# Kernel tuning notes

Hardware: AMD Instinct MI355X
Metric: run time of the kernel (lower is better)

## Reference

```python
import jax, jax.numpy as jnp
import numpy as np

N_NODES = 100000
N_EDGES = 1000000
N_GRAPHS = 512
HID = 64
EDIM = 32
LAYERS = 4
BN_EPS = 1e-5


def _batchnorm(x, g, b):
    # training-mode BatchNorm1d: biased batch statistics over the node axis
    m = x.mean(axis=0)
    v = jnp.var(x, axis=0)
    return (x - m) * jax.lax.rsqrt(v + BN_EPS) * g + b


def setup_inputs() -> dict:
    key = jax.random.key(0)
    ks = jax.random.split(key, 16)
    zw = 2 * HID + EDIM  # 160: cat([x_i, x_j, e_ij])
    inp = {
        "z": jax.random.randint(ks[0], (N_NODES,), 0, 100),
        "edge_index": jax.random.randint(ks[1], (2, N_EDGES), 0, N_NODES),
        "edge_attr": jax.random.normal(ks[2], (N_EDGES, EDIM), dtype=jnp.float32),
        "batch_ids": jnp.sort(jax.random.randint(ks[3], (N_NODES,), 0, N_GRAPHS)),
        "emb": jax.random.normal(ks[4], (100, HID), dtype=jnp.float32),
        "Wf": jax.random.normal(ks[5], (LAYERS, zw, HID), dtype=jnp.float32) / np.sqrt(zw),
        "bf": jnp.zeros((LAYERS, HID), jnp.float32),
        "Ws": jax.random.normal(ks[6], (LAYERS, zw, HID), dtype=jnp.float32) / np.sqrt(zw),
        "bs": jnp.zeros((LAYERS, HID), jnp.float32),
        "g_cbn": jnp.ones((LAYERS, HID), jnp.float32),
        "b_cbn": jnp.zeros((LAYERS, HID), jnp.float32),
        "g_obn": jnp.ones((LAYERS, HID), jnp.float32),
        "b_obn": jnp.zeros((LAYERS, HID), jnp.float32),
        "W1": jax.random.normal(ks[7], (HID, HID), dtype=jnp.float32) / np.sqrt(HID),
        "b1": jnp.zeros((HID,), jnp.float32),
        "W2": jax.random.normal(ks[8], (HID, 1), dtype=jnp.float32) / np.sqrt(HID),
        "b2": jnp.zeros((1,), jnp.float32),
    }
    return inp


def reference(z, edge_index, edge_attr, batch_ids, emb, Wf, bf, Ws, bs,
              g_cbn, b_cbn, g_obn, b_obn, W1, b1, W2, b2):
    src = edge_index[0]  # x_j (source)
    dst = edge_index[1]  # x_i (target / aggregation index)
    x = emb[z]  # [N, HID]
    for l in range(LAYERS):
        # CGConv message: z_e = cat([x_i, x_j, e_ij]); m = sigmoid(f(z_e)) * softplus(s(z_e))
        z_e = jnp.concatenate([x[dst], x[src], edge_attr], axis=-1)  # [E, 160]
        msg = jax.nn.sigmoid(z_e @ Wf[l] + bf[l]) * jax.nn.softplus(z_e @ Ws[l] + bs[l])
        agg = jax.ops.segment_sum(msg, dst, num_segments=N_NODES)  # [N, HID]
        agg = _batchnorm(agg, g_cbn[l], b_cbn[l])  # CGConv's internal BN
        x = agg + x  # residual
        x = _batchnorm(x, g_obn[l], b_obn[l])  # outer BatchNorm1d
        x = jax.nn.softplus(x)
    # global mean pool over graphs
    sums = jax.ops.segment_sum(x, batch_ids, num_segments=N_GRAPHS)
    cnts = jax.ops.segment_sum(jnp.ones((N_NODES,), x.dtype), batch_ids, num_segments=N_GRAPHS)
    pooled = sums / jnp.maximum(cnts, 1.0)[:, None]
    h = jax.nn.silu(pooled @ W1 + b1)  # dropout is identity in eval mode
    out = (h @ W2 + b2)[:, 0]
    return out
```

## Files before the change

### kernel.cpp

```cpp
#include <hip/hip_runtime.h>
#include <cstdint>
#include <cstddef>

#define N_NODES 100000
#define N_EDGES 1000000
#define N_GRAPHS 512
#define HID 64
#define EDIM 32
#define LAYERS 4
#define BN_EPS 1e-5

static const size_t X_OFF    = 0;
static const size_t AGG_OFF  = X_OFF + 25600000;
static const size_t STA_OFF  = AGG_OFF + 25600000;
static const size_t STB_OFF  = STA_OFF + 1024;
static const size_t POOL_OFF = STB_OFF + 1024;
static const size_t CNT_OFF  = POOL_OFF + 131072;
static const size_t DEG_OFF  = CNT_OFF + 2048;
static const size_t ECUR_OFF = DEG_OFF + 400128;
static const size_t PERM_OFF = ECUR_OFF + 400128;
static const size_t DSTS_OFF = PERM_OFF + 4000000;
static const size_t BSUM_OFF = DSTS_OFF + 4000000;
static const size_t BOFF_OFF = BSUM_OFF + 2048;
static const size_t P_OFF    = BOFF_OFF + 2048;

#define SCAN_BLOCKS 391

__device__ __forceinline__ float rl_f(float v, int k) {
    return __uint_as_float(__builtin_amdgcn_readlane(__float_as_uint(v), k));
}
__device__ __forceinline__ float sigmoidf_(float x) {
    return 1.f / (1.f + __expf(-x));
}
__device__ __forceinline__ float softplusf_(float x) {
    return fmaxf(x, 0.f) + __logf(1.f + __expf(-fabsf(x)));
}
__device__ __forceinline__ void fma4(float4& a, const float4& wv, float xv) {
    a.x = fmaf(xv, wv.x, a.x);
    a.y = fmaf(xv, wv.y, a.y);
    a.z = fmaf(xv, wv.z, a.z);
    a.w = fmaf(xv, wv.w, a.w);
}

__global__ __launch_bounds__(256) void cg_embed(const int* __restrict__ z,
                                                const float* __restrict__ emb,
                                                float* __restrict__ x) {
    int i = blockIdx.x * 256 + threadIdx.x;
    if (i < N_NODES * HID) {
        x[i] = emb[z[i >> 6] * HID + (i & 63)];
    }
}

__global__ __launch_bounds__(256) void cg_hist(const int* __restrict__ ei,
                                               int* __restrict__ deg) {
    int e = blockIdx.x * 256 + threadIdx.x;
    if (e < N_EDGES) atomicAdd(&deg[ei[N_EDGES + e]], 1);
}

__global__ __launch_bounds__(256) void cg_bsum(const int* __restrict__ deg,
                                               int* __restrict__ bsum) {
    const int i = blockIdx.x * 256 + threadIdx.x;
    int v = (i < N_NODES) ? deg[i] : 0;
#pragma unroll
    for (int off = 32; off > 0; off >>= 1) v += __shfl_down(v, off);
    __shared__ int wsum[4];
    if ((threadIdx.x & 63) == 0) wsum[threadIdx.x >> 6] = v;
    __syncthreads();
    if (threadIdx.x == 0) bsum[blockIdx.x] = wsum[0] + wsum[1] + wsum[2] + wsum[3];
}

__global__ __launch_bounds__(512) void cg_bscan(const int* __restrict__ bsum,
                                                int* __restrict__ boff) {
    __shared__ int ps[512];
    const int t = threadIdx.x;
    int v = (t < SCAN_BLOCKS) ? bsum[t] : 0;
    ps[t] = v;
    __syncthreads();
    for (int off = 1; off < 512; off <<= 1) {
        int u = (t >= off) ? ps[t - off] : 0;
        __syncthreads();
        ps[t] += u;
        __syncthreads();
    }
    if (t < SCAN_BLOCKS) boff[t] = ps[t] - v;
}

__global__ __launch_bounds__(256) void cg_escan(const int* __restrict__ deg,
                                                const int* __restrict__ boff,
                                                int* __restrict__ ecur) {
    __shared__ int ps[256];
    const int t = threadIdx.x;
    const int i = blockIdx.x * 256 + t;
    int v = (i < N_NODES) ? deg[i] : 0;
    ps[t] = v;
    __syncthreads();
    for (int off = 1; off < 256; off <<= 1) {
        int u = (t >= off) ? ps[t - off] : 0;
        __syncthreads();
        ps[t] += u;
        __syncthreads();
    }
    if (i < N_NODES) ecur[i] = ps[t] - v + boff[blockIdx.x];
}

__global__ __launch_bounds__(256) void cg_scatter(const int* __restrict__ ei,
                                                  int* __restrict__ ecur,
                                                  int* __restrict__ perm,
                                                  int* __restrict__ dst_s) {
    int e = blockIdx.x * 256 + threadIdx.x;
    if (e < N_EDGES) {
        int d = ei[N_EDGES + e];
        int pos = atomicAdd(&ecur[d], 1);
        perm[pos] = e;
        dst_s[pos] = d;
    }
}

__global__ __launch_bounds__(256, 4) void cg_nodeP4(const float* __restrict__ x,
                                                    const float* __restrict__ Wf,
                                                    const float* __restrict__ Ws,
                                                    float* __restrict__ P) {
    __shared__ __align__(16) float xs[64][68];
    const int tid = threadIdx.x;
    const int base = blockIdx.x * 64;
#pragma unroll
    for (int i = 0; i < 4; i++) {
        int f4 = tid * 4 + i;
        int r = f4 >> 4, c4 = (f4 & 15) * 4;
        float4 v = {0, 0, 0, 0};
        if (base + r < N_NODES) v = *(const float4*)(x + (size_t)(base + r) * HID + c4);
        *(float4*)(&xs[r][c4]) = v;
    }
    __syncthreads();

    const int g = tid >> 4;
    const int j4 = (tid & 15) * 4;
    float4 acc[4][4];
#pragma unroll
    for (int m = 0; m < 4; m++)
#pragma unroll
        for (int q = 0; q < 4; q++) acc[m][q] = {0, 0, 0, 0};

    for (int k = 0; k < 64; k++) {
        float4 w0 = *(const float4*)(Wf + (size_t)k * HID + j4);
        float4 w1 = *(const float4*)(Ws + (size_t)k * HID + j4);
        float4 w2 = *(const float4*)(Wf + (size_t)(64 + k) * HID + j4);
        float4 w3 = *(const float4*)(Ws + (size_t)(64 + k) * HID + j4);
#pragma unroll
        for (int m = 0; m < 4; m++) {
            float xv = xs[g + m * 16][k];
            fma4(acc[m][0], w0, xv);
            fma4(acc[m][1], w1, xv);
            fma4(acc[m][2], w2, xv);
            fma4(acc[m][3], w3, xv);
        }
    }
#pragma unroll
    for (int m = 0; m < 4; m++) {
        int r = base + g + m * 16;
        if (r < N_NODES) {
            float* o = P + (size_t)r * 256;
            *(float4*)(o + j4)       = acc[m][0];
            *(float4*)(o + 64 + j4)  = acc[m][1];
            *(float4*)(o + 128 + j4) = acc[m][2];
            *(float4*)(o + 192 + j4) = acc[m][3];
        }
    }
}

__global__ __launch_bounds__(256, 4) void cg_edge3(const float* __restrict__ P,
                                                   const int* __restrict__ ei,
                                                   const float* __restrict__ ea,
                                                   const int* __restrict__ perm,
                                                   const int* __restrict__ dst_s,
                                                   const float* __restrict__ WfE,
                                                   const float* __restrict__ WsE,
                                                   const float* __restrict__ bf,
                                                   const float* __restrict__ bs,
                                                   float* __restrict__ agg) {
    const int j = threadIdx.x & 63;
    float wfe[EDIM], wse[EDIM];
#pragma unroll
    for (int k = 0; k < EDIM; k++) {
        wfe[k] = WfE[k * HID + j];
        wse[k] = WsE[k * HID + j];
    }
    const float bfv = bf[j], bsv = bs[j];
    const int wave = blockIdx.x * 4 + (threadIdx.x >> 6);
    const int nw = gridDim.x * 4;
    const int chunk = (N_EDGES + nw - 1) / nw;
    const int e0 = wave * chunk;
    const int e1 = min(e0 + chunk, N_EDGES);
    if (e0 >= e1) return;

    int cur = __builtin_amdgcn_readfirstlane(dst_s[e0]);
    float pf0 = P[(size_t)cur * 256 + j];
    float ps0 = P[(size_t)cur * 256 + 64 + j];
    float acc = 0.f;

    for (int e = e0; e < e1; ++e) {
        const int d  = __builtin_amdgcn_readfirstlane(dst_s[e]);
        const int pe = __builtin_amdgcn_readfirstlane(perm[e]);
        if (d != cur) {
            unsafeAtomicAdd(&agg[(size_t)cur * HID + j], acc);
            acc = 0.f;
            cur = d;
            pf0 = P[(size_t)cur * 256 + j];
            ps0 = P[(size_t)cur * 256 + 64 + j];
        }
        const int s = __builtin_amdgcn_readfirstlane(ei[pe]);
        const float sf = P[(size_t)s * 256 + 128 + j];
        const float ss = P[(size_t)s * 256 + 192 + j];
        const float* __restrict__ earow = ea + (size_t)pe * EDIM;
        float uf = bfv + pf0 + sf;
        float us = bsv + ps0 + ss;
#pragma unroll
        for (int k = 0; k < EDIM; k++) {
            const float ek = earow[k];
            uf = fmaf(ek, wfe[k], uf);
            us = fmaf(ek, wse[k], us);
        }
        acc += sigmoidf_(uf) * softplusf_(us);
    }
    unsafeAtomicAdd(&agg[(size_t)cur * HID + j], acc);
}

__global__ __launch_bounds__(256) void cg_stats(const float* __restrict__ a,
                                                double* __restrict__ stA,
                                                double* __restrict__ stB) {
    if (blockIdx.x == 0 && threadIdx.x < 128) stB[threadIdx.x] = 0.0;
    const int j = threadIdx.x & 63, rl = threadIdx.x >> 6;
    float s = 0.f, q = 0.f;
    for (int n = blockIdx.x * 4 + rl; n < N_NODES; n += gridDim.x * 4) {
        float v = a[(size_t)n * HID + j];
        s += v;
        q += v * v;
    }
    __shared__ float ls[4][64], lq[4][64];
    ls[rl][j] = s;
    lq[rl][j] = q;
    __syncthreads();
    if (threadIdx.x < 64) {
        float S = ls[0][j] + ls[1][j] + ls[2][j] + ls[3][j];
        float Q = lq[0][j] + lq[1][j] + lq[2][j] + lq[3][j];
        unsafeAtomicAdd(&stA[j], (double)S);
        unsafeAtomicAdd(&stA[64 + j], (double)Q);
    }
}

__global__ __launch_bounds__(256) void cg_bn1res(float* __restrict__ agg,
                                                 const float* __restrict__ x,
                                                 const float* __restrict__ g,
                                                 const float* __restrict__ b,
                                                 const double* __restrict__ stA,
                                                 double* __restrict__ stB) {
    const int j = threadIdx.x & 63, rl = threadIdx.x >> 6;
    const double mean = stA[j] * (1.0 / N_NODES);
    const double var  = stA[64 + j] * (1.0 / N_NODES) - mean * mean;
    const float sc = (float)((double)g[j] / sqrt(var + BN_EPS));
    const float sh = (float)((double)b[j] - mean * (double)sc);
    float s = 0.f, q = 0.f;
    for (int n = blockIdx.x * 4 + rl; n < N_NODES; n += gridDim.x * 4) {
        size_t idx = (size_t)n * HID + j;
        float v = fmaf(agg[idx], sc, sh) + x[idx];
        agg[idx] = v;
        s += v;
        q += v * v;
    }
    __shared__ float ls[4][64], lq[4][64];
    ls[rl][j] = s;
    lq[rl][j] = q;
    __syncthreads();
    if (threadIdx.x < 64) {
        float S = ls[0][j] + ls[1][j] + ls[2][j] + ls[3][j];
        float Q = lq[0][j] + lq[1][j] + lq[2][j] + lq[3][j];
        unsafeAtomicAdd(&stB[j], (double)S);
        unsafeAtomicAdd(&stB[64 + j], (double)Q);
    }
}

__global__ __launch_bounds__(256) void cg_bn2act(float* __restrict__ agg,
                                                 float* __restrict__ x,
                                                 const float* __restrict__ g,
                                                 const float* __restrict__ b,
                                                 const double* __restrict__ stB,
                                                 double* __restrict__ stA) {
    if (blockIdx.x == 0 && threadIdx.x < 128) stA[threadIdx.x] = 0.0;
    const int j = threadIdx.x & 63, rl = threadIdx.x >> 6;
    const double mean = stB[j] * (1.0 / N_NODES);
    const double var  = stB[64 + j] * (1.0 / N_NODES) - mean * mean;
    const float sc = (float)((double)g[j] / sqrt(var + BN_EPS));
    const float sh = (float)((double)b[j] - mean * (double)sc);
    for (int n = blockIdx.x * 4 + rl; n < N_NODES; n += gridDim.x * 4) {
        size_t idx = (size_t)n * HID + j;
        x[idx] = softplusf_(fmaf(agg[idx], sc, sh));
        agg[idx] = 0.f;
    }
}

__global__ __launch_bounds__(256) void cg_pool(const float* __restrict__ x,
                                               const int* __restrict__ bid,
                                               float* __restrict__ pooled,
                                               float* __restrict__ cnt) {
    const int j = threadIdx.x & 63, rl = threadIdx.x >> 6;
    const int chunk = (N_NODES + gridDim.x - 1) / gridDim.x;
    const int s0 = blockIdx.x * chunk;
    const int e0 = min(s0 + chunk, N_NODES);
    float acc = 0.f, c = 0.f;
    int cur = -1;
    for (int n = s0 + rl; n < e0; n += 4) {
        int bg = bid[n];
        if (bg != cur) {
            if (cur >= 0) {
                unsafeAtomicAdd(&pooled[(size_t)cur * HID + j], acc);
                if (j == 0) unsafeAtomicAdd(&cnt[cur], c);
            }
            cur = bg;
            acc = 0.f;
            c = 0.f;
        }
        acc += x[(size_t)n * HID + j];
        c += 1.f;
    }
    if (cur >= 0) {
        unsafeAtomicAdd(&pooled[(size_t)cur * HID + j], acc);
        if (j == 0) unsafeAtomicAdd(&cnt[cur], c);
    }
}

__global__ __launch_bounds__(64) void cg_mlp(const float* __restrict__ pooled,
                                             const float* __restrict__ cnt,
                                             const float* __restrict__ W1,
                                             const float* __restrict__ b1,
                                             const float* __restrict__ W2,
                                             const float* __restrict__ b2,
                                             float* __restrict__ out) {
    const int g = blockIdx.x;
    const int j = threadIdx.x;
    const float c = fmaxf(cnt[g], 1.f);
    const float p = pooled[(size_t)g * HID + j] / c;
    float h = b1[j];
    for (int k = 0; k < HID; k++) {
        h = fmaf(rl_f(p, k), W1[k * HID + j], h);
    }
    const float hs = h * sigmoidf_(h);
    float v = hs * W2[j];
#pragma unroll
    for (int off = 32; off > 0; off >>= 1) v += __shfl_down(v, off);
    if (j == 0) out[g] = v + b2[0];
}

extern "C" void kernel_launch(void* const* d_in, const int* in_sizes, int n_in,
                              void* d_out, int out_size, void* d_ws, size_t ws_size,
                              hipStream_t stream) {
    const int*   z   = (const int*)d_in[0];
    const int*   ei  = (const int*)d_in[1];
    const float* ea  = (const float*)d_in[2];
    const int*   bid = (const int*)d_in[3];
    const float* emb = (const float*)d_in[4];
    const float* Wf  = (const float*)d_in[5];
    const float* bf  = (const float*)d_in[6];
    const float* Ws  = (const float*)d_in[7];
    const float* bs  = (const float*)d_in[8];
    const float* gc  = (const float*)d_in[9];
    const float* bc  = (const float*)d_in[10];
    const float* go  = (const float*)d_in[11];
    const float* bo  = (const float*)d_in[12];
    const float* W1  = (const float*)d_in[13];
    const float* b1  = (const float*)d_in[14];
    const float* W2  = (const float*)d_in[15];
    const float* b2  = (const float*)d_in[16];
    float* out = (float*)d_out;

    char* ws = (char*)d_ws;
    float*  x      = (float*)(ws + X_OFF);
    float*  agg    = (float*)(ws + AGG_OFF);
    double* stA    = (double*)(ws + STA_OFF);
    double* stB    = (double*)(ws + STB_OFF);
    float*  pooled = (float*)(ws + POOL_OFF);
    float*  cnt    = (float*)(ws + CNT_OFF);
    int*    deg    = (int*)(ws + DEG_OFF);
    int*    ecur   = (int*)(ws + ECUR_OFF);
    int*    perm   = (int*)(ws + PERM_OFF);
    int*    dst_s  = (int*)(ws + DSTS_OFF);
    int*    bsum   = (int*)(ws + BSUM_OFF);
    int*    boff   = (int*)(ws + BOFF_OFF);
    float*  P      = (float*)(ws + P_OFF);

    (void)hipMemsetAsync(ws + AGG_OFF, 0, 25600000 + 2048, stream);
    (void)hipMemsetAsync(ws + POOL_OFF, 0, 131072 + 2048, stream);
    (void)hipMemsetAsync(ws + DEG_OFF, 0, 400000, stream);

    cg_hist<<<(N_EDGES + 255) / 256, 256, 0, stream>>>(ei, deg);
    cg_bsum<<<SCAN_BLOCKS, 256, 0, stream>>>(deg, bsum);
    cg_bscan<<<1, 512, 0, stream>>>(bsum, boff);
    cg_escan<<<SCAN_BLOCKS, 256, 0, stream>>>(deg, boff, ecur);
    cg_scatter<<<(N_EDGES + 255) / 256, 256, 0, stream>>>(ei, ecur, perm, dst_s);

    cg_embed<<<(N_NODES * HID + 255) / 256, 256, 0, stream>>>(z, emb, x);

    for (int l = 0; l < LAYERS; l++) {
        const float* Wfl = Wf + (size_t)l * 160 * HID;
        const float* Wsl = Ws + (size_t)l * 160 * HID;
        cg_nodeP4<<<(N_NODES + 63) / 64, 256, 0, stream>>>(x, Wfl, Wsl, P);
        cg_edge3<<<2048, 256, 0, stream>>>(P, ei, ea, perm, dst_s,
                                           Wfl + 128 * HID, Wsl + 128 * HID,
                                           bf + l * HID, bs + l * HID, agg);
        cg_stats<<<1024, 256, 0, stream>>>(agg, stA, stB);
        cg_bn1res<<<1024, 256, 0, stream>>>(agg, x, gc + l * HID, bc + l * HID, stA, stB);
        cg_bn2act<<<1024, 256, 0, stream>>>(agg, x, go + l * HID, bo + l * HID, stB, stA);
    }

    cg_pool<<<1024, 256, 0, stream>>>(x, bid, pooled, cnt);
    cg_mlp<<<N_GRAPHS, 64, 0, stream>>>(pooled, cnt, W1, b1, W2, b2, out);
}
```

Before: 2.398 ms.

## Prefetch next edge in edge kernel, presort src ids, replace double atomics with partials

The scatter pass now also writes source ids in sorted order, so the edge kernel no longer does a dependent ei[perm] lookup. The edge loop software-prefetches the next edge's indices and source P rows, loads the edge-attribute row up front, and splits the FMA chains in two for more ILP. Grid size drops to 1024 blocks and nodeP4 occupancy hint changes to 2. BatchNorm statistics switch from double atomics to per-block float partials reduced by a single-block finalize kernel, which adds two small launches per layer.

```diff
diff --git a/kernel.cpp b/kernel.cpp
--- a/kernel.cpp
+++ b/kernel.cpp
@@ -9,20 +9,23 @@
 #define EDIM 32
 #define LAYERS 4
 #define BN_EPS 1e-5
+#define NPB 1024
 
 static const size_t X_OFF    = 0;
-static const size_t AGG_OFF  = X_OFF + 25600000;
-static const size_t STA_OFF  = AGG_OFF + 25600000;
-static const size_t STB_OFF  = STA_OFF + 1024;
-static const size_t POOL_OFF = STB_OFF + 1024;
-static const size_t CNT_OFF  = POOL_OFF + 131072;
-static const size_t DEG_OFF  = CNT_OFF + 2048;
-static const size_t ECUR_OFF = DEG_OFF + 400128;
-static const size_t PERM_OFF = ECUR_OFF + 400128;
-static const size_t DSTS_OFF = PERM_OFF + 4000000;
-static const size_t BSUM_OFF = DSTS_OFF + 4000000;
-static const size_t BOFF_OFF = BSUM_OFF + 2048;
-static const size_t P_OFF    = BOFF_OFF + 2048;
+static const size_t AGG_OFF  = 25600000;
+static const size_t STA_OFF  = 51200000;
+static const size_t STB_OFF  = 51201024;
+static const size_t POOL_OFF = 51202048;
+static const size_t CNT_OFF  = 51333120;
+static const size_t DEG_OFF  = 51335168;
+static const size_t ECUR_OFF = 51735296;
+static const size_t PERM_OFF = 52135424;
+static const size_t DSTS_OFF = 56135424;
+static const size_t SRCS_OFF = 60135424;
+static const size_t BSUM_OFF = 64135424;
+static const size_t BOFF_OFF = 64137472;
+static const size_t PART_OFF = 64139520;
+static const size_t P_OFF    = 64663808;
 
 #define SCAN_BLOCKS 391
 
@@ -106,17 +109,19 @@
 __global__ __launch_bounds__(256) void cg_scatter(const int* __restrict__ ei,
                                                   int* __restrict__ ecur,
                                                   int* __restrict__ perm,
-                                                  int* __restrict__ dst_s) {
+                                                  int* __restrict__ dst_s,
+                                                  int* __restrict__ src_s) {
     int e = blockIdx.x * 256 + threadIdx.x;
     if (e < N_EDGES) {
         int d = ei[N_EDGES + e];
         int pos = atomicAdd(&ecur[d], 1);
         perm[pos] = e;
         dst_s[pos] = d;
-    }
-}
-
-__global__ __launch_bounds__(256, 4) void cg_nodeP4(const float* __restrict__ x,
+        src_s[pos] = ei[e];
+    }
+}
+
+__global__ __launch_bounds__(256, 2) void cg_nodeP4(const float* __restrict__ x,
                                                     const float* __restrict__ Wf,
                                                     const float* __restrict__ Ws,
                                                     float* __restrict__ P) {
@@ -168,11 +173,11 @@
     }
 }
 
-__global__ __launch_bounds__(256, 4) void cg_edge3(const float* __restrict__ P,
-                                                   const int* __restrict__ ei,
+__global__ __launch_bounds__(256, 4) void cg_edge4(const float* __restrict__ P,
                                                    const float* __restrict__ ea,
                                                    const int* __restrict__ perm,
                                                    const int* __restrict__ dst_s,
+                                                   const int* __restrict__ src_s,
                                                    const float* __restrict__ WfE,
                                                    const float* __restrict__ WsE,
                                                    const float* __restrict__ bf,
@@ -181,11 +186,16 @@
     const int j = threadIdx.x & 63;
     float wfe[EDIM], wse[EDIM];
 #pragma unroll
+    for (int k = 0; k < EDIM; k++) wfe[k] = WfE[k * HID + j];
+#pragma unroll
+    for (int k = 0; k < EDIM; k++) wse[k] = WsE[k * HID + j];
+#pragma unroll
     for (int k = 0; k < EDIM; k++) {
-        wfe[k] = WfE[k * HID + j];
-        wse[k] = WsE[k * HID + j];
+        asm volatile("" : "+v"(wfe[k]));
+        asm volatile("" : "+v"(wse[k]));
     }
     const float bfv = bf[j], bsv = bs[j];
+
     const int wave = blockIdx.x * 4 + (threadIdx.x >> 6);
     const int nw = gridDim.x * 4;
     const int chunk = (N_EDGES + nw - 1) / nw;
@@ -193,14 +203,34 @@
     const int e1 = min(e0 + chunk, N_EDGES);
     if (e0 >= e1) return;
 
-    int cur = __builtin_amdgcn_readfirstlane(dst_s[e0]);
+    int eu = __builtin_amdgcn_readfirstlane(e0);
+    int d_c  = dst_s[eu];
+    int s_c  = src_s[eu];
+    int pe_c = perm[eu];
+    float sf_c = P[(size_t)s_c * 256 + 128 + j];
+    float ss_c = P[(size_t)s_c * 256 + 192 + j];
+
+    int cur = __builtin_amdgcn_readfirstlane(d_c);
     float pf0 = P[(size_t)cur * 256 + j];
     float ps0 = P[(size_t)cur * 256 + 64 + j];
     float acc = 0.f;
 
     for (int e = e0; e < e1; ++e) {
-        const int d  = __builtin_amdgcn_readfirstlane(dst_s[e]);
-        const int pe = __builtin_amdgcn_readfirstlane(perm[e]);
+        const int d  = __builtin_amdgcn_readfirstlane(d_c);
+        const int pe = __builtin_amdgcn_readfirstlane(pe_c);
+        const float sf = sf_c, ss = ss_c;
+        const float* __restrict__ er = ea + (size_t)pe * EDIM;
+        float e_r[EDIM];
+#pragma unroll
+        for (int k = 0; k < EDIM; k++) e_r[k] = er[k];
+        if (e + 1 < e1) {
+            int nu = __builtin_amdgcn_readfirstlane(e + 1);
+            d_c  = dst_s[nu];
+            s_c  = src_s[nu];
+            pe_c = perm[nu];
+            sf_c = P[(size_t)s_c * 256 + 128 + j];
+            ss_c = P[(size_t)s_c * 256 + 192 + j];
+        }
         if (d != cur) {
             unsafeAtomicAdd(&agg[(size_t)cur * HID + j], acc);
             acc = 0.f;
@@ -208,27 +238,22 @@
             pf0 = P[(size_t)cur * 256 + j];
             ps0 = P[(size_t)cur * 256 + 64 + j];
         }
-        const int s = __builtin_amdgcn_readfirstlane(ei[pe]);
-        const float sf = P[(size_t)s * 256 + 128 + j];
-        const float ss = P[(size_t)s * 256 + 192 + j];
-        const float* __restrict__ earow = ea + (size_t)pe * EDIM;
-        float uf = bfv + pf0 + sf;
-        float us = bsv + ps0 + ss;
-#pragma unroll
-        for (int k = 0; k < EDIM; k++) {
-            const float ek = earow[k];
-            uf = fmaf(ek, wfe[k], uf);
-            us = fmaf(ek, wse[k], us);
-        }
-        acc += sigmoidf_(uf) * softplusf_(us);
+        float uf0 = bfv + pf0, uf1 = sf;
+        float us0 = bsv + ps0, us1 = ss;
+#pragma unroll
+        for (int k = 0; k < EDIM; k += 2) {
+            uf0 = fmaf(e_r[k], wfe[k], uf0);
+            us0 = fmaf(e_r[k], wse[k], us0);
+            uf1 = fmaf(e_r[k + 1], wfe[k + 1], uf1);
+            us1 = fmaf(e_r[k + 1], wse[k + 1], us1);
+        }
+        acc += sigmoidf_(uf0 + uf1) * softplusf_(us0 + us1);
     }
     unsafeAtomicAdd(&agg[(size_t)cur * HID + j], acc);
 }
 
 __global__ __launch_bounds__(256) void cg_stats(const float* __restrict__ a,
-                                                double* __restrict__ stA,
-                                                double* __restrict__ stB) {
-    if (blockIdx.x == 0 && threadIdx.x < 128) stB[threadIdx.x] = 0.0;
+                                                float* __restrict__ parts) {
     const int j = threadIdx.x & 63, rl = threadIdx.x >> 6;
     float s = 0.f, q = 0.f;
     for (int n = blockIdx.x * 4 + rl; n < N_NODES; n += gridDim.x * 4) {
@@ -243,9 +268,22 @@
     if (threadIdx.x < 64) {
         float S = ls[0][j] + ls[1][j] + ls[2][j] + ls[3][j];
         float Q = lq[0][j] + lq[1][j] + lq[2][j] + lq[3][j];
-        unsafeAtomicAdd(&stA[j], (double)S);
-        unsafeAtomicAdd(&stA[64 + j], (double)Q);
-    }
+        parts[(size_t)blockIdx.x * 128 + j] = S;
+        parts[(size_t)blockIdx.x * 128 + 64 + j] = Q;
+    }
+}
+
+__global__ __launch_bounds__(256) void cg_fin(const float* __restrict__ parts,
+                                              double* __restrict__ st) {
+    const int c = threadIdx.x & 127;
+    const int h = threadIdx.x >> 7;
+    double s = 0.0;
+    for (int i = h * (NPB / 2); i < (h + 1) * (NPB / 2); i++)
+        s += (double)parts[(size_t)i * 128 + c];
+    __shared__ double sh[128];
+    if (h == 0) sh[c] = s;
+    __syncthreads();
+    if (h == 1) st[c] = sh[c] + s;
 }
 
 __global__ __launch_bounds__(256) void cg_bn1res(float* __restrict__ agg,
@@ -253,7 +291,7 @@
                                                  const float* __restrict__ g,
                                                  const float* __restrict__ b,
                                                  const double* __restrict__ stA,
-                                                 double* __restrict__ stB) {
+                                                 float* __restrict__ parts) {
     const int j = threadIdx.x & 63, rl = threadIdx.x >> 6;
     const double mean = stA[j] * (1.0 / N_NODES);
     const double var  = stA[64 + j] * (1.0 / N_NODES) - mean * mean;
@@ -274,8 +312,8 @@
     if (threadIdx.x < 64) {
         float S = ls[0][j] + ls[1][j] + ls[2][j] + ls[3][j];
         float Q = lq[0][j] + lq[1][j] + lq[2][j] + lq[3][j];
-        unsafeAtomicAdd(&stB[j], (double)S);
-        unsafeAtomicAdd(&stB[64 + j], (double)Q);
+        parts[(size_t)blockIdx.x * 128 + j] = S;
+        parts[(size_t)blockIdx.x * 128 + 64 + j] = Q;
     }
 }
 
@@ -283,9 +321,7 @@
                                                  float* __restrict__ x,
                                                  const float* __restrict__ g,
                                                  const float* __restrict__ b,
-                                                 const double* __restrict__ stB,
-                                                 double* __restrict__ stA) {
-    if (blockIdx.x == 0 && threadIdx.x < 128) stA[threadIdx.x] = 0.0;
+                                                 const double* __restrict__ stB) {
     const int j = threadIdx.x & 63, rl = threadIdx.x >> 6;
     const double mean = stB[j] * (1.0 / N_NODES);
     const double var  = stB[64 + j] * (1.0 / N_NODES) - mean * mean;
@@ -383,11 +419,13 @@
     int*    ecur   = (int*)(ws + ECUR_OFF);
     int*    perm   = (int*)(ws + PERM_OFF);
     int*    dst_s  = (int*)(ws + DSTS_OFF);
+    int*    src_s  = (int*)(ws + SRCS_OFF);
     int*    bsum   = (int*)(ws + BSUM_OFF);
     int*    boff   = (int*)(ws + BOFF_OFF);
+    float*  parts  = (float*)(ws + PART_OFF);
     float*  P      = (float*)(ws + P_OFF);
 
-    (void)hipMemsetAsync(ws + AGG_OFF, 0, 25600000 + 2048, stream);
+    (void)hipMemsetAsync(ws + AGG_OFF, 0, 25600000, stream);
     (void)hipMemsetAsync(ws + POOL_OFF, 0, 131072 + 2048, stream);
     (void)hipMemsetAsync(ws + DEG_OFF, 0, 400000, stream);
 
@@ -395,7 +433,7 @@
     cg_bsum<<<SCAN_BLOCKS, 256, 0, stream>>>(deg, bsum);
     cg_bscan<<<1, 512, 0, stream>>>(bsum, boff);
     cg_escan<<<SCAN_BLOCKS, 256, 0, stream>>>(deg, boff, ecur);
-    cg_scatter<<<(N_EDGES + 255) / 256, 256, 0, stream>>>(ei, ecur, perm, dst_s);
+    cg_scatter<<<(N_EDGES + 255) / 256, 256, 0, stream>>>(ei, ecur, perm, dst_s, src_s);
 
     cg_embed<<<(N_NODES * HID + 255) / 256, 256, 0, stream>>>(z, emb, x);
 
@@ -403,12 +441,14 @@
         const float* Wfl = Wf + (size_t)l * 160 * HID;
         const float* Wsl = Ws + (size_t)l * 160 * HID;
         cg_nodeP4<<<(N_NODES + 63) / 64, 256, 0, stream>>>(x, Wfl, Wsl, P);
-        cg_edge3<<<2048, 256, 0, stream>>>(P, ei, ea, perm, dst_s,
+        cg_edge4<<<1024, 256, 0, stream>>>(P, ea, perm, dst_s, src_s,
                                            Wfl + 128 * HID, Wsl + 128 * HID,
                                            bf + l * HID, bs + l * HID, agg);
-        cg_stats<<<1024, 256, 0, stream>>>(agg, stA, stB);
-        cg_bn1res<<<1024, 256, 0, stream>>>(agg, x, gc + l * HID, bc + l * HID, stA, stB);
-        cg_bn2act<<<1024, 256, 0, stream>>>(agg, x, go + l * HID, bo + l * HID, stB, stA);
+        cg_stats<<<NPB, 256, 0, stream>>>(agg, parts);
+        cg_fin<<<1, 256, 0, stream>>>(parts, stA);
+        cg_bn1res<<<NPB, 256, 0, stream>>>(agg, x, gc + l * HID, bc + l * HID, stA, parts);
+        cg_fin<<<1, 256, 0, stream>>>(parts, stB);
+        cg_bn2act<<<NPB, 256, 0, stream>>>(agg, x, go + l * HID, bo + l * HID, stB);
     }
 
     cg_pool<<<1024, 256, 0, stream>>>(x, bid, pooled, cnt);
```

Measured after the change: 2.203 ms. 8.1% less time.
